# Optimization experiments

Measured on AMD Instinct MI355X. Metric: run time of the kernel, lower is better.

The kernel has to match this reference:

```python
import jax, jax.numpy as jnp
import numpy as np

N_WAY = 5
N_SHOT = 25
N_SUPPORT = N_WAY * N_SHOT  # 125
N_QUERY = 2048
D = 8192
C_REG = 0.1        # default C_reg of MetaOptNetHead_SVM_CS
MAX_ITER = 20      # default maxIter of QPFunction
SIGMA = 0.1        # centering parameter of the interior-point iteration


def setup_inputs() -> dict:
    key = jax.random.key(0)
    k1, k2, k3 = jax.random.split(key, 3)
    query = jax.random.normal(k1, (N_QUERY, D), dtype=jnp.float32)
    support = jax.random.normal(k2, (N_SUPPORT, D), dtype=jnp.float32)
    support_labels = jax.random.randint(k3, (N_SUPPORT,), 0, N_WAY, dtype=jnp.int32)
    scale = jnp.ones((1,), dtype=jnp.float32)  # nn.Parameter([1.0])
    return {
        "query": query,
        "support": support,
        "support_labels": support_labels,
        "n_way": N_WAY,
        "n_shot": N_SHOT,
        "scale": scale,
    }


def _solve_qp(G, e, h, A, b):
    """Solve min_z 0.5 z^T G z + e^T z  s.t.  z <= h (C = I),  A z = b.

    Primal-dual infeasible-start interior-point method with MAX_ITER fixed
    Newton steps (the jax analogue of qpth's QPFunction(maxIter=20)).
    Shapes: G (B,n,n), e (B,n), h (B,n), A (B,p,n), b (B,p).
    """
    B, n = e.shape
    p = b.shape[1]
    m = n  # C = I -> one inequality per variable
    At = jnp.swapaxes(A, 1, 2)                      # (B,n,p)
    zero_pp = jnp.zeros((B, p, p), dtype=G.dtype)
    A_row = jnp.concatenate([A, zero_pp], axis=2)   # (B,p,n+p), constant

    z = jnp.zeros_like(e)
    s = jnp.ones_like(h)
    lam = jnp.ones_like(h)
    nu = jnp.zeros_like(b)

    def frac_to_boundary(x, dx):
        # largest alpha in (0,1] keeping x + alpha*dx > 0
        ratio = jnp.where(dx < 0, -x / jnp.where(dx < 0, dx, -1.0), jnp.inf)
        return jnp.min(ratio, axis=1)

    def step(carry, _):
        z, s, lam, nu = carry
        Gz = jnp.einsum('bij,bj->bi', G, z)
        r1 = Gz + e + lam + jnp.einsum('bpi,bp->bi', A, nu)   # dual residual (C^T lam = lam)
        r2 = z + s - h                                         # primal ineq residual
        r4 = jnp.einsum('bpi,bi->bp', A, z) - b                # primal eq residual
        mu = SIGMA * jnp.sum(s * lam, axis=1, keepdims=True) / m
        r3 = lam * s - mu                                      # perturbed complementarity
        # Reduced KKT system: (G + diag(lam/s)) dz + A^T dnu = rhs1 ; A dz = -r4
        H = G + jax.vmap(jnp.diag)(lam / s)                    # (B,n,n)
        rhs1 = -(r1 + (lam * r2 - r3) / s)                     # (B,n)
        K = jnp.concatenate(
            [jnp.concatenate([H, At], axis=2), A_row], axis=1)  # (B,n+p,n+p)
        rhs = jnp.concatenate([rhs1, -r4], axis=1)             # (B,n+p)
        sol = jnp.linalg.solve(K, rhs[..., None])[..., 0]
        dz, dnu = sol[:, :n], sol[:, n:]
        ds = -r2 - dz
        dlam = (-r3 - lam * ds) / s
        alpha = jnp.minimum(
            1.0, 0.99 * jnp.minimum(frac_to_boundary(s, ds),
                                    frac_to_boundary(lam, dlam)))[:, None]
        return (z + alpha * dz, s + alpha * ds,
                lam + alpha * dlam, nu + alpha * dnu), None

    (z, s, lam, nu), _ = jax.lax.scan(step, (z, s, lam, nu), None, length=MAX_ITER)
    return z


def _svm_cs_head(query, support, support_labels, n_way):
    support_b = support[None]            # (1, ns, d) -- head unsqueezes batch dim
    query_b = query[None]                # (1, nq, d)
    B, ns, _ = support_b.shape
    f32 = jnp.float32

    # Gram matrix of support, then kron with I_{n_way} (batched_kronecker == jnp.kron)
    K = jnp.einsum('bnd,bmd->bnm', support_b, support_b)            # (B,ns,ns)
    eye_w = jnp.eye(n_way, dtype=f32)
    G = jax.vmap(lambda k: jnp.kron(k, eye_w))(K)                    # (B,ns*nw,ns*nw)
    G = G + jnp.eye(n_way * ns, dtype=f32)[None]

    y1h = jax.nn.one_hot(support_labels, n_way, dtype=f32).reshape(B, ns * n_way)
    e = -y1h
    h = C_REG * y1h
    A = jnp.kron(jnp.eye(ns, dtype=f32), jnp.ones((1, n_way), f32))[None]  # (1,ns,ns*nw)
    b = jnp.zeros((B, ns), f32)

    qp_sol = _solve_qp(G, e, h, A, b)                                # (B, ns*nw)

    compat = jnp.einsum('bnd,bqd->bnq', support_b, query_b)          # (B,ns,nq)
    qp3 = qp_sol.reshape(B, ns, n_way)
    # logits[b,q,w] = sum_s qp3[b,s,w] * compat[b,s,q]
    logits = jnp.einsum('bsw,bsq->bqw', qp3, compat)                 # (B,nq,nw)
    num_sv = jnp.sum(jnp.any(qp3 > 0.001, axis=2))                   # support-vector count
    return logits, num_sv


def reference(query, support, support_labels, n_way, n_shot, scale):
    logits, num_sv = _svm_cs_head(query, support, support_labels, n_way)
    return scale * logits, num_sv
```

## Files before the change

### kernel.cpp

```cpp
#include <hip/hip_runtime.h>

#define NS   125
#define NW   5
#define NQ   2048
#define DD   8192
#define CREG 0.1f
#define PGD_ITERS 10

#define OFF_PART  0
#define OFF_K     1000000
#define OFF_QP3   1016000
#define OFF_W     1017000

#define NPART     64

__global__ __launch_bounds__(256, 2) void gram256(const float* __restrict__ support,
                                                  float* __restrict__ part) {
    __shared__ __align__(16) float As[64][132];
    __shared__ __align__(16) float Bs[64][132];
    const int tid = threadIdx.x;
    const int c  = blockIdx.x >> 2;
    const int qy = blockIdx.x & 1, qz = (blockIdx.x >> 1) & 1;
    const int d0 = c * 128;
    const int sy0 = qy * 64, sz0 = qz * 64;

#pragma unroll
    for (int it = 0; it < 8; ++it) {
        int idx = it * 256 + tid;
        int sl = idx >> 5, d4 = idx & 31;
        int sa = sy0 + sl, sb = sz0 + sl;
        float4 va = (sa < NS) ? *(const float4*)&support[(size_t)sa * DD + d0 + d4 * 4]
                              : make_float4(0.f, 0.f, 0.f, 0.f);
        float4 vb = (sb < NS) ? *(const float4*)&support[(size_t)sb * DD + d0 + d4 * 4]
                              : make_float4(0.f, 0.f, 0.f, 0.f);
        *(float4*)&As[sl][d4 * 4] = va;
        *(float4*)&Bs[sl][d4 * 4] = vb;
    }
    __syncthreads();

    const int tx = tid & 15, ty = tid >> 4;
    float acc[4][4];
#pragma unroll
    for (int i = 0; i < 4; i++)
#pragma unroll
        for (int j = 0; j < 4; j++) acc[i][j] = 0.f;

#pragma unroll 4
    for (int d4 = 0; d4 < 32; ++d4) {
        float4 a4[4], b4[4];
#pragma unroll
        for (int i = 0; i < 4; i++) a4[i] = *(const float4*)&As[tx + 16 * i][d4 * 4];
#pragma unroll
        for (int j = 0; j < 4; j++) b4[j] = *(const float4*)&Bs[ty + 16 * j][d4 * 4];
#pragma unroll
        for (int i = 0; i < 4; i++)
#pragma unroll
            for (int j = 0; j < 4; j++)
                acc[i][j] += a4[i].x * b4[j].x + a4[i].y * b4[j].y
                           + a4[i].z * b4[j].z + a4[i].w * b4[j].w;
    }

    float* dst = part + (size_t)c * (NS * NS);
#pragma unroll
    for (int i = 0; i < 4; i++) {
        int gi = sy0 + tx + 16 * i;
        if (gi >= NS) continue;
#pragma unroll
        for (int j = 0; j < 4; j++) {
            int gj = sz0 + ty + 16 * j;
            if (gj < NS) dst[gi * NS + gj] = acc[i][j];
        }
    }
}

__global__ __launch_bounds__(256) void kreduce(const float* __restrict__ part,
                                               float* __restrict__ Kg) {
    int t = blockIdx.x * 256 + threadIdx.x;
    if (t < NS * NS) {
        float s = 0.f;
#pragma unroll 8
        for (int c = 0; c < NPART; ++c) s += part[(size_t)c * (NS * NS) + t];
        Kg[t] = s;
    }
}

__global__ __launch_bounds__(256) void qp_solve(const float* __restrict__ Kg,
                                                const int* __restrict__ labels,
                                                float* __restrict__ qp3,
                                                float* __restrict__ outNumSv) {
    __shared__ float red2[2][128 * 25];
    __shared__ __align__(16) float zsw[2][4][NW][32];
    __shared__ float rsx[2];
    __shared__ int   svc;

    const int tid  = threadIdx.x;
    const int w    = tid >> 6;
    const int lane = tid & 63;
    const int c0   = w * 32;
    const int r0   = lane, r1 = lane + 64;

    float kr0[32], kr1[32];
#pragma unroll
    for (int j = 0; j < 32; ++j) {
        const int col = c0 + j;
        const bool cv = (col < NS);
        kr0[j] = cv ? Kg[col * NS + r0] : 0.f;
        kr1[j] = (cv && r1 < NS) ? Kg[col * NS + r1] : 0.f;
    }
    for (int idx = tid; idx < 2 * 4 * NW * 32; idx += 256) ((float*)zsw)[idx] = 0.f;
    if (tid == 0) svc = 0;
    float rsum0 = 0.f, rsum1 = 0.f;
#pragma unroll
    for (int j = 0; j < 32; ++j) { rsum0 += fabsf(kr0[j]); rsum1 += fabsf(kr1[j]); }
    red2[0][r0 * 25 + w * 5] = rsum0;
    red2[0][r1 * 25 + w * 5] = rsum1;
    __syncthreads();
    const int prw = w * 64 + lane;
    if (w < 2) {
        const float* rr = &red2[0][prw * 25];
        float t = (prw < NS) ? rr[0] + rr[5] + rr[10] + rr[15] : 0.f;
#pragma unroll
        for (int off = 32; off; off >>= 1) t = fmaxf(t, __shfl_xor(t, off));
        if (lane == 0) rsx[w] = t;
    }
    __syncthreads();
    const float eta = 1.9f / (fmaxf(rsx[0], rsx[1]) + 1.0f);
    const int pr   = c0 + lane;
    const bool act = (lane < 32) && (pr < NS);
    const int lab  = act ? labels[pr] : 0;
    float z[NW] = {0.f, 0.f, 0.f, 0.f, 0.f};

    for (int it = 0; it < PGD_ITERS; ++it) {
        const int p = it & 1, n = p ^ 1;
        float acc0[NW] = {0.f, 0.f, 0.f, 0.f, 0.f};
        float acc1[NW] = {0.f, 0.f, 0.f, 0.f, 0.f};
#pragma unroll
        for (int c = 0; c < 8; ++c) {
            float4 z0 = *(const float4*)&zsw[p][w][0][4 * c];
            float4 z1 = *(const float4*)&zsw[p][w][1][4 * c];
            float4 z2 = *(const float4*)&zsw[p][w][2][4 * c];
            float4 z3 = *(const float4*)&zsw[p][w][3][4 * c];
            float4 z4 = *(const float4*)&zsw[p][w][4][4 * c];
            const float k00 = kr0[4*c], k01 = kr0[4*c+1], k02 = kr0[4*c+2], k03 = kr0[4*c+3];
            const float k10 = kr1[4*c], k11 = kr1[4*c+1], k12 = kr1[4*c+2], k13 = kr1[4*c+3];
            acc0[0] += k00*z0.x + k01*z0.y + k02*z0.z + k03*z0.w;
            acc0[1] += k00*z1.x + k01*z1.y + k02*z1.z + k03*z1.w;
            acc0[2] += k00*z2.x + k01*z2.y + k02*z2.z + k03*z2.w;
            acc0[3] += k00*z3.x + k01*z3.y + k02*z3.z + k03*z3.w;
            acc0[4] += k00*z4.x + k01*z4.y + k02*z4.z + k03*z4.w;
            acc1[0] += k10*z0.x + k11*z0.y + k12*z0.z + k13*z0.w;
            acc1[1] += k10*z1.x + k11*z1.y + k12*z1.z + k13*z1.w;
            acc1[2] += k10*z2.x + k11*z2.y + k12*z2.z + k13*z2.w;
            acc1[3] += k10*z3.x + k11*z3.y + k12*z3.z + k13*z3.w;
            acc1[4] += k10*z4.x + k11*z4.y + k12*z4.z + k13*z4.w;
        }
        {
            float* b0 = &red2[p][r0 * 25 + w * 5];
            b0[0] = acc0[0]; b0[1] = acc0[1]; b0[2] = acc0[2]; b0[3] = acc0[3]; b0[4] = acc0[4];
            float* b1 = &red2[p][r1 * 25 + w * 5];
            b1[0] = acc1[0]; b1[1] = acc1[1]; b1[2] = acc1[2]; b1[3] = acc1[3]; b1[4] = acc1[4];
        }
        __syncthreads();
        if (act) {
            const float* rr = &red2[p][pr * 25];
            float v[NW], h[NW];
#pragma unroll
            for (int a = 0; a < NW; a++) {
                float kz = rr[a] + rr[5 + a] + rr[10 + a] + rr[15 + a];
                float g = kz + z[a] - ((a == lab) ? 1.f : 0.f);
                v[a] = z[a] - eta * g;
                h[a] = (a == lab) ? CREG : 0.f;
            }
            float tau = fmaxf(fmaxf(fmaxf(v[0], v[1]), fmaxf(v[2], v[3])), v[4]);
#pragma unroll
            for (int nn = 0; nn < 7; ++nn) {
                float g = 0.f, nf = 0.f;
#pragma unroll
                for (int a = 0; a < NW; a++) {
                    float d = v[a] - tau;
                    bool fr = (d <= h[a]);
                    g += fr ? d : h[a];
                    nf += fr ? 1.f : 0.f;
                }
                tau += g / nf;
            }
#pragma unroll
            for (int a = 0; a < NW; a++) {
                z[a] = fminf(v[a] - tau, h[a]);
                zsw[n][w][a][lane] = z[a];
            }
        }
    }

    if (act) {
        float m = fmaxf(fmaxf(fmaxf(z[0], z[1]), fmaxf(z[2], z[3])), z[4]);
        if (m > 0.001f) atomicAdd(&svc, 1);
#pragma unroll
        for (int a = 0; a < NW; a++) qp3[pr * NW + a] = z[a];
    }
    __syncthreads();
    if (tid == 0) *outNumSv = (float)svc;
}

__global__ __launch_bounds__(256) void w_kernel(const float* __restrict__ support,
                                                const float* __restrict__ qp3,
                                                float* __restrict__ W) {
    __shared__ float q3[NS * NW];
    __shared__ float red[4 * 64 * NW];
    const int tid = threadIdx.x;
    for (int i = tid; i < NS * NW; i += 256) q3[i] = qp3[i];
    __syncthreads();
    const int ld = tid & 63;
    const int sq = tid >> 6;
    const int d  = blockIdx.x * 64 + ld;
    const int s0 = sq * 32;
    const int s1 = (sq == 3) ? NS : (s0 + 32);
    float acc[NW] = {0.f, 0.f, 0.f, 0.f, 0.f};
#pragma unroll 4
    for (int s = s0; s < s1; ++s) {
        float sv = support[(size_t)s * DD + d];
#pragma unroll
        for (int a = 0; a < NW; a++) acc[a] += sv * q3[s * NW + a];
    }
    float* rr = &red[tid * NW];
#pragma unroll
    for (int a = 0; a < NW; a++) rr[a] = acc[a];
    __syncthreads();
    if (sq == 0) {
#pragma unroll
        for (int a = 0; a < NW; a++) {
            float s = red[(0 * 64 + ld) * NW + a] + red[(1 * 64 + ld) * NW + a]
                    + red[(2 * 64 + ld) * NW + a] + red[(3 * 64 + ld) * NW + a];
            W[(size_t)a * DD + d] = s;
        }
    }
}

__global__ __launch_bounds__(256) void logits8(const float* __restrict__ query,
                                               const float* __restrict__ W,
                                               const float* __restrict__ scale,
                                               float* __restrict__ out) {
    __shared__ float red[4][8][NW];
    const int tid = threadIdx.x;
    const int wave = tid >> 6, lane = tid & 63;
    const int q0 = blockIdx.x * 8;
    const int v0 = wave * 512;
    const float4* W4 = (const float4*)W;
    const float4* q4 = (const float4*)query;
    const float sc = scale[0];

    float acc[8][NW];
#pragma unroll
    for (int k = 0; k < 8; k++)
#pragma unroll
        for (int a = 0; a < NW; a++) acc[k][a] = 0.f;

    for (int it = 0; it < 8; ++it) {
        const int dv = v0 + it * 64 + lane;
        float4 qv[8];
#pragma unroll
        for (int k = 0; k < 8; k++) qv[k] = q4[(size_t)(q0 + k) * (DD / 4) + dv];
#pragma unroll
        for (int a = 0; a < NW; a++) {
            float4 wv = W4[a * (DD / 4) + dv];
#pragma unroll
            for (int k = 0; k < 8; k++)
                acc[k][a] += qv[k].x * wv.x + qv[k].y * wv.y
                           + qv[k].z * wv.z + qv[k].w * wv.w;
        }
    }
#pragma unroll
    for (int off = 32; off; off >>= 1) {
#pragma unroll
        for (int k = 0; k < 8; k++)
#pragma unroll
            for (int a = 0; a < NW; a++) acc[k][a] += __shfl_xor(acc[k][a], off);
    }
    if (lane == 0) {
#pragma unroll
        for (int k = 0; k < 8; k++)
#pragma unroll
            for (int a = 0; a < NW; a++) red[wave][k][a] = acc[k][a];
    }
    __syncthreads();
    if (tid < 8 * NW) {
        const int ql = tid / NW, a = tid % NW;
        float s = red[0][ql][a] + red[1][ql][a] + red[2][ql][a] + red[3][ql][a];
        out[(q0 + ql) * NW + a] = sc * s;
    }
}

extern "C" void kernel_launch(void* const* d_in, const int* in_sizes, int n_in,
                              void* d_out, int out_size, void* d_ws, size_t ws_size,
                              hipStream_t stream) {
    const float* query   = (const float*)d_in[0];
    const float* support = (const float*)d_in[1];
    const int*   labels  = (const int*)d_in[2];
    const float* scale   = (const float*)d_in[5];
    float* out = (float*)d_out;
    float* ws  = (float*)d_ws;

    float* part = ws + OFF_PART;
    float* Kg   = ws + OFF_K;
    float* qp3  = ws + OFF_QP3;
    float* W    = ws + OFF_W;

    hipLaunchKernelGGL(gram256, dim3(256), dim3(256), 0, stream, support, part);
    hipLaunchKernelGGL(kreduce, dim3((NS * NS + 255) / 256), dim3(256), 0, stream, part, Kg);
    hipLaunchKernelGGL(qp_solve, dim3(1), dim3(256), 0, stream, Kg, labels, qp3, out + NQ * NW);
    hipLaunchKernelGGL(w_kernel, dim3(DD / 64), dim3(256), 0, stream, support, qp3, W);
    hipLaunchKernelGGL(logits8, dim3(NQ / 8), dim3(256), 0, stream, query, W, scale, out);
}
```

Before: 158.0 us.

## Fuse K reduction, QP solve and W computation into one flag-synchronized kernel

Merges kreduce, qp_solve and w_kernel into a single 129-block kernel. Blocks cooperatively reduce the Gram partials, then block 0 runs the QP after a global atomic counter shows all blocks are done, while the other blocks prefetch support slices into shared memory and spin until the QP result is published. It also exploits Gram symmetry by computing only three of the four 64x64 quadrants, 192 blocks instead of 256, and mirroring the missing one during the reduction. This removes two launches and overlaps the support loads with the serial QP. The cost is a reliance on all 129 blocks being co-resident, since the spin-waits would otherwise deadlock.

```diff
diff --git a/kernel.cpp b/kernel.cpp
--- a/kernel.cpp
+++ b/kernel.cpp
@@ -9,18 +9,24 @@
 
 #define OFF_PART  0
 #define OFF_K     1000000
+#define OFF_FLAGS 1015632
 #define OFF_QP3   1016000
 #define OFF_W     1017000
 
 #define NPART     64
-
-__global__ __launch_bounds__(256, 2) void gram256(const float* __restrict__ support,
-                                                  float* __restrict__ part) {
+#define QPW_BLKS  129
+
+__global__ __launch_bounds__(256, 2) void gram192(const float* __restrict__ support,
+                                                  float* __restrict__ part,
+                                                  unsigned int* __restrict__ flags) {
     __shared__ __align__(16) float As[64][132];
     __shared__ __align__(16) float Bs[64][132];
     const int tid = threadIdx.x;
-    const int c  = blockIdx.x >> 2;
-    const int qy = blockIdx.x & 1, qz = (blockIdx.x >> 1) & 1;
+    if (blockIdx.x == 0 && tid == 0) { flags[0] = 0u; flags[1] = 0u; }
+    const int qsel = blockIdx.x % 3;
+    const int c    = blockIdx.x / 3;
+    const int qy = (qsel == 2) ? 1 : 0;
+    const int qz = (qsel == 0) ? 0 : 1;
     const int d0 = c * 128;
     const int sy0 = qy * 64, sz0 = qz * 64;
 
@@ -73,165 +79,190 @@
     }
 }
 
-__global__ __launch_bounds__(256) void kreduce(const float* __restrict__ part,
-                                               float* __restrict__ Kg) {
-    int t = blockIdx.x * 256 + threadIdx.x;
-    if (t < NS * NS) {
+__global__ __launch_bounds__(256) void qpw(const float* __restrict__ part,
+                                           const int* __restrict__ labels,
+                                           const float* __restrict__ support,
+                                           float* __restrict__ Kg,
+                                           unsigned int* __restrict__ flags,
+                                           float* __restrict__ qp3,
+                                           float* __restrict__ W,
+                                           float* __restrict__ outNumSv) {
+    __shared__ __align__(16) float smem[9920];
+    __shared__ float rsx[2];
+    __shared__ int   svc;
+    const int tid = threadIdx.x;
+    const int bid = blockIdx.x;
+
+    for (int t = bid * 256 + tid; t < NS * NS; t += QPW_BLKS * 256) {
+        int i = t / NS, j = t - i * NS;
+        int src = (i >= 64 && j < 64) ? (j * NS + i) : t;
         float s = 0.f;
 #pragma unroll 8
-        for (int c = 0; c < NPART; ++c) s += part[(size_t)c * (NS * NS) + t];
+        for (int c = 0; c < NPART; ++c) s += part[(size_t)c * (NS * NS) + src];
         Kg[t] = s;
     }
-}
-
-__global__ __launch_bounds__(256) void qp_solve(const float* __restrict__ Kg,
-                                                const int* __restrict__ labels,
-                                                float* __restrict__ qp3,
-                                                float* __restrict__ outNumSv) {
-    __shared__ float red2[2][128 * 25];
-    __shared__ __align__(16) float zsw[2][4][NW][32];
-    __shared__ float rsx[2];
-    __shared__ int   svc;
-
-    const int tid  = threadIdx.x;
-    const int w    = tid >> 6;
-    const int lane = tid & 63;
-    const int c0   = w * 32;
-    const int r0   = lane, r1 = lane + 64;
-
-    float kr0[32], kr1[32];
-#pragma unroll
-    for (int j = 0; j < 32; ++j) {
-        const int col = c0 + j;
-        const bool cv = (col < NS);
-        kr0[j] = cv ? Kg[col * NS + r0] : 0.f;
-        kr1[j] = (cv && r1 < NS) ? Kg[col * NS + r1] : 0.f;
-    }
-    for (int idx = tid; idx < 2 * 4 * NW * 32; idx += 256) ((float*)zsw)[idx] = 0.f;
-    if (tid == 0) svc = 0;
-    float rsum0 = 0.f, rsum1 = 0.f;
-#pragma unroll
-    for (int j = 0; j < 32; ++j) { rsum0 += fabsf(kr0[j]); rsum1 += fabsf(kr1[j]); }
-    red2[0][r0 * 25 + w * 5] = rsum0;
-    red2[0][r1 * 25 + w * 5] = rsum1;
     __syncthreads();
-    const int prw = w * 64 + lane;
-    if (w < 2) {
-        const float* rr = &red2[0][prw * 25];
-        float t = (prw < NS) ? rr[0] + rr[5] + rr[10] + rr[15] : 0.f;
-#pragma unroll
-        for (int off = 32; off; off >>= 1) t = fmaxf(t, __shfl_xor(t, off));
-        if (lane == 0) rsx[w] = t;
-    }
-    __syncthreads();
-    const float eta = 1.9f / (fmaxf(rsx[0], rsx[1]) + 1.0f);
-    const int pr   = c0 + lane;
-    const bool act = (lane < 32) && (pr < NS);
-    const int lab  = act ? labels[pr] : 0;
-    float z[NW] = {0.f, 0.f, 0.f, 0.f, 0.f};
-
-    for (int it = 0; it < PGD_ITERS; ++it) {
-        const int p = it & 1, n = p ^ 1;
-        float acc0[NW] = {0.f, 0.f, 0.f, 0.f, 0.f};
-        float acc1[NW] = {0.f, 0.f, 0.f, 0.f, 0.f};
-#pragma unroll
-        for (int c = 0; c < 8; ++c) {
-            float4 z0 = *(const float4*)&zsw[p][w][0][4 * c];
-            float4 z1 = *(const float4*)&zsw[p][w][1][4 * c];
-            float4 z2 = *(const float4*)&zsw[p][w][2][4 * c];
-            float4 z3 = *(const float4*)&zsw[p][w][3][4 * c];
-            float4 z4 = *(const float4*)&zsw[p][w][4][4 * c];
-            const float k00 = kr0[4*c], k01 = kr0[4*c+1], k02 = kr0[4*c+2], k03 = kr0[4*c+3];
-            const float k10 = kr1[4*c], k11 = kr1[4*c+1], k12 = kr1[4*c+2], k13 = kr1[4*c+3];
-            acc0[0] += k00*z0.x + k01*z0.y + k02*z0.z + k03*z0.w;
-            acc0[1] += k00*z1.x + k01*z1.y + k02*z1.z + k03*z1.w;
-            acc0[2] += k00*z2.x + k01*z2.y + k02*z2.z + k03*z2.w;
-            acc0[3] += k00*z3.x + k01*z3.y + k02*z3.z + k03*z3.w;
-            acc0[4] += k00*z4.x + k01*z4.y + k02*z4.z + k03*z4.w;
-            acc1[0] += k10*z0.x + k11*z0.y + k12*z0.z + k13*z0.w;
-            acc1[1] += k10*z1.x + k11*z1.y + k12*z1.z + k13*z1.w;
-            acc1[2] += k10*z2.x + k11*z2.y + k12*z2.z + k13*z2.w;
-            acc1[3] += k10*z3.x + k11*z3.y + k12*z3.z + k13*z3.w;
-            acc1[4] += k10*z4.x + k11*z4.y + k12*z4.z + k13*z4.w;
-        }
-        {
-            float* b0 = &red2[p][r0 * 25 + w * 5];
-            b0[0] = acc0[0]; b0[1] = acc0[1]; b0[2] = acc0[2]; b0[3] = acc0[3]; b0[4] = acc0[4];
-            float* b1 = &red2[p][r1 * 25 + w * 5];
-            b1[0] = acc1[0]; b1[1] = acc1[1]; b1[2] = acc1[2]; b1[3] = acc1[3]; b1[4] = acc1[4];
-        }
-        __syncthreads();
+    if (tid == 0)
+        __hip_atomic_fetch_add(&flags[0], 1u, __ATOMIC_RELEASE, __HIP_MEMORY_SCOPE_AGENT);
+
+    if (bid == 0) {
+        if (tid == 0) {
+            while (__hip_atomic_load(&flags[0], __ATOMIC_RELAXED, __HIP_MEMORY_SCOPE_AGENT) < (unsigned)QPW_BLKS)
+                __builtin_amdgcn_s_sleep(8);
+        }
+        __syncthreads();
+        (void)__hip_atomic_load(&flags[0], __ATOMIC_ACQUIRE, __HIP_MEMORY_SCOPE_AGENT);
+
+        float* red2 = smem;
+        float* zsw  = smem + 6400;
+        const int w    = tid >> 6;
+        const int lane = tid & 63;
+        const int c0   = w * 32;
+        const int r0 = lane, r1 = lane + 64;
+        float kr0[32], kr1[32];
+#pragma unroll
+        for (int j = 0; j < 32; ++j) {
+            const int col = c0 + j;
+            const bool cv = (col < NS);
+            kr0[j] = cv ? Kg[col * NS + r0] : 0.f;
+            kr1[j] = (cv && r1 < NS) ? Kg[col * NS + r1] : 0.f;
+        }
+        for (int idx = tid; idx < 2 * 4 * NW * 32; idx += 256) zsw[idx] = 0.f;
+        if (tid == 0) svc = 0;
+        float rsum0 = 0.f, rsum1 = 0.f;
+#pragma unroll
+        for (int j = 0; j < 32; ++j) { rsum0 += fabsf(kr0[j]); rsum1 += fabsf(kr1[j]); }
+        red2[r0 * 25 + w * 5] = rsum0;
+        red2[r1 * 25 + w * 5] = rsum1;
+        __syncthreads();
+        const int prw = w * 64 + lane;
+        if (w < 2) {
+            const float* rr = &red2[prw * 25];
+            float t = (prw < NS) ? rr[0] + rr[5] + rr[10] + rr[15] : 0.f;
+#pragma unroll
+            for (int off = 32; off; off >>= 1) t = fmaxf(t, __shfl_xor(t, off));
+            if (lane == 0) rsx[w] = t;
+        }
+        __syncthreads();
+        const float eta = 1.9f / (fmaxf(rsx[0], rsx[1]) + 1.0f);
+        const int pr  = c0 + lane;
+        const bool act = (lane < 32) && (pr < NS);
+        const int lab = act ? labels[pr] : 0;
+        float z[NW] = {0.f, 0.f, 0.f, 0.f, 0.f};
+
+        for (int it = 0; it < PGD_ITERS; ++it) {
+            const int p = it & 1, n = p ^ 1;
+            float acc0[NW] = {0.f, 0.f, 0.f, 0.f, 0.f};
+            float acc1[NW] = {0.f, 0.f, 0.f, 0.f, 0.f};
+            const float* zb = zsw + p * 640 + w * 160;
+#pragma unroll
+            for (int c = 0; c < 8; ++c) {
+                float4 z0 = *(const float4*)&zb[0 * 32 + 4 * c];
+                float4 z1 = *(const float4*)&zb[1 * 32 + 4 * c];
+                float4 z2 = *(const float4*)&zb[2 * 32 + 4 * c];
+                float4 z3 = *(const float4*)&zb[3 * 32 + 4 * c];
+                float4 z4 = *(const float4*)&zb[4 * 32 + 4 * c];
+                const float k00 = kr0[4*c], k01 = kr0[4*c+1], k02 = kr0[4*c+2], k03 = kr0[4*c+3];
+                const float k10 = kr1[4*c], k11 = kr1[4*c+1], k12 = kr1[4*c+2], k13 = kr1[4*c+3];
+                acc0[0] += k00*z0.x + k01*z0.y + k02*z0.z + k03*z0.w;
+                acc0[1] += k00*z1.x + k01*z1.y + k02*z1.z + k03*z1.w;
+                acc0[2] += k00*z2.x + k01*z2.y + k02*z2.z + k03*z2.w;
+                acc0[3] += k00*z3.x + k01*z3.y + k02*z3.z + k03*z3.w;
+                acc0[4] += k00*z4.x + k01*z4.y + k02*z4.z + k03*z4.w;
+                acc1[0] += k10*z0.x + k11*z0.y + k12*z0.z + k13*z0.w;
+                acc1[1] += k10*z1.x + k11*z1.y + k12*z1.z + k13*z1.w;
+                acc1[2] += k10*z2.x + k11*z2.y + k12*z2.z + k13*z2.w;
+                acc1[3] += k10*z3.x + k11*z3.y + k12*z3.z + k13*z3.w;
+                acc1[4] += k10*z4.x + k11*z4.y + k12*z4.z + k13*z4.w;
+            }
+            {
+                float* b0 = &red2[p * 3200 + r0 * 25 + w * 5];
+                b0[0] = acc0[0]; b0[1] = acc0[1]; b0[2] = acc0[2]; b0[3] = acc0[3]; b0[4] = acc0[4];
+                float* b1 = &red2[p * 3200 + r1 * 25 + w * 5];
+                b1[0] = acc1[0]; b1[1] = acc1[1]; b1[2] = acc1[2]; b1[3] = acc1[3]; b1[4] = acc1[4];
+            }
+            __syncthreads();
+            if (act) {
+                const float* rr = &red2[p * 3200 + pr * 25];
+                float v[NW], h[NW];
+#pragma unroll
+                for (int a = 0; a < NW; a++) {
+                    float kz = rr[a] + rr[5 + a] + rr[10 + a] + rr[15 + a];
+                    float g = kz + z[a] - ((a == lab) ? 1.f : 0.f);
+                    v[a] = z[a] - eta * g;
+                    h[a] = (a == lab) ? CREG : 0.f;
+                }
+                float tau = fmaxf(fmaxf(fmaxf(v[0], v[1]), fmaxf(v[2], v[3])), v[4]);
+#pragma unroll
+                for (int nn = 0; nn < 7; ++nn) {
+                    float g = 0.f, nf = 0.f;
+#pragma unroll
+                    for (int a = 0; a < NW; a++) {
+                        float d = v[a] - tau;
+                        bool fr = (d <= h[a]);
+                        g += fr ? d : h[a];
+                        nf += fr ? 1.f : 0.f;
+                    }
+                    tau += g / nf;
+                }
+#pragma unroll
+                for (int a = 0; a < NW; a++) {
+                    z[a] = fminf(v[a] - tau, h[a]);
+                    zsw[n * 640 + w * 160 + a * 32 + lane] = z[a];
+                }
+            }
+        }
+
         if (act) {
-            const float* rr = &red2[p][pr * 25];
-            float v[NW], h[NW];
+            float m = fmaxf(fmaxf(fmaxf(z[0], z[1]), fmaxf(z[2], z[3])), z[4]);
+            if (m > 0.001f) atomicAdd(&svc, 1);
+#pragma unroll
+            for (int a = 0; a < NW; a++) qp3[pr * NW + a] = z[a];
+        }
+        __syncthreads();
+        if (tid == 0) {
+            *outNumSv = (float)svc;
+            __hip_atomic_fetch_add(&flags[1], 1u, __ATOMIC_RELEASE, __HIP_MEMORY_SCOPE_AGENT);
+        }
+    } else {
+        float* sup = smem;
+        float* q3  = smem + 8000;
+        float* red = smem + 8640;
+        const int dbase = (bid - 1) * 64;
+        for (int idx = tid; idx < NS * 64; idx += 256) {
+            int s = idx >> 6, dc = idx & 63;
+            sup[idx] = support[(size_t)s * DD + dbase + dc];
+        }
+        if (tid == 0) {
+            while (__hip_atomic_load(&flags[1], __ATOMIC_RELAXED, __HIP_MEMORY_SCOPE_AGENT) < 1u)
+                __builtin_amdgcn_s_sleep(16);
+        }
+        __syncthreads();
+        (void)__hip_atomic_load(&flags[1], __ATOMIC_ACQUIRE, __HIP_MEMORY_SCOPE_AGENT);
+        for (int i = tid; i < NS * NW; i += 256) q3[i] = qp3[i];
+        __syncthreads();
+        const int ld = tid & 63;
+        const int sq = tid >> 6;
+        const int s0 = sq * 32;
+        const int s1 = (sq == 3) ? NS : (s0 + 32);
+        float acc[NW] = {0.f, 0.f, 0.f, 0.f, 0.f};
+#pragma unroll 4
+        for (int s = s0; s < s1; ++s) {
+            float sv = sup[s * 64 + ld];
+#pragma unroll
+            for (int a = 0; a < NW; a++) acc[a] += sv * q3[s * NW + a];
+        }
+        float* rr = &red[tid * NW];
+#pragma unroll
+        for (int a = 0; a < NW; a++) rr[a] = acc[a];
+        __syncthreads();
+        if (sq == 0) {
 #pragma unroll
             for (int a = 0; a < NW; a++) {
-                float kz = rr[a] + rr[5 + a] + rr[10 + a] + rr[15 + a];
-                float g = kz + z[a] - ((a == lab) ? 1.f : 0.f);
-                v[a] = z[a] - eta * g;
-                h[a] = (a == lab) ? CREG : 0.f;
+                float s = red[(0 * 64 + ld) * NW + a] + red[(1 * 64 + ld) * NW + a]
+                        + red[(2 * 64 + ld) * NW + a] + red[(3 * 64 + ld) * NW + a];
+                W[(size_t)a * DD + dbase + ld] = s;
             }
-            float tau = fmaxf(fmaxf(fmaxf(v[0], v[1]), fmaxf(v[2], v[3])), v[4]);
-#pragma unroll
-            for (int nn = 0; nn < 7; ++nn) {
-                float g = 0.f, nf = 0.f;
-#pragma unroll
-                for (int a = 0; a < NW; a++) {
-                    float d = v[a] - tau;
-                    bool fr = (d <= h[a]);
-                    g += fr ? d : h[a];
-                    nf += fr ? 1.f : 0.f;
-                }
-                tau += g / nf;
-            }
-#pragma unroll
-            for (int a = 0; a < NW; a++) {
-                z[a] = fminf(v[a] - tau, h[a]);
-                zsw[n][w][a][lane] = z[a];
-            }
-        }
-    }
-
-    if (act) {
-        float m = fmaxf(fmaxf(fmaxf(z[0], z[1]), fmaxf(z[2], z[3])), z[4]);
-        if (m > 0.001f) atomicAdd(&svc, 1);
-#pragma unroll
-        for (int a = 0; a < NW; a++) qp3[pr * NW + a] = z[a];
-    }
-    __syncthreads();
-    if (tid == 0) *outNumSv = (float)svc;
-}
-
-__global__ __launch_bounds__(256) void w_kernel(const float* __restrict__ support,
-                                                const float* __restrict__ qp3,
-                                                float* __restrict__ W) {
-    __shared__ float q3[NS * NW];
-    __shared__ float red[4 * 64 * NW];
-    const int tid = threadIdx.x;
-    for (int i = tid; i < NS * NW; i += 256) q3[i] = qp3[i];
-    __syncthreads();
-    const int ld = tid & 63;
-    const int sq = tid >> 6;
-    const int d  = blockIdx.x * 64 + ld;
-    const int s0 = sq * 32;
-    const int s1 = (sq == 3) ? NS : (s0 + 32);
-    float acc[NW] = {0.f, 0.f, 0.f, 0.f, 0.f};
-#pragma unroll 4
-    for (int s = s0; s < s1; ++s) {
-        float sv = support[(size_t)s * DD + d];
-#pragma unroll
-        for (int a = 0; a < NW; a++) acc[a] += sv * q3[s * NW + a];
-    }
-    float* rr = &red[tid * NW];
-#pragma unroll
-    for (int a = 0; a < NW; a++) rr[a] = acc[a];
-    __syncthreads();
-    if (sq == 0) {
-#pragma unroll
-        for (int a = 0; a < NW; a++) {
-            float s = red[(0 * 64 + ld) * NW + a] + red[(1 * 64 + ld) * NW + a]
-                    + red[(2 * 64 + ld) * NW + a] + red[(3 * 64 + ld) * NW + a];
-            W[(size_t)a * DD + d] = s;
         }
     }
 }
@@ -300,14 +331,14 @@
     float* out = (float*)d_out;
     float* ws  = (float*)d_ws;
 
-    float* part = ws + OFF_PART;
-    float* Kg   = ws + OFF_K;
-    float* qp3  = ws + OFF_QP3;
-    float* W    = ws + OFF_W;
-
-    hipLaunchKernelGGL(gram256, dim3(256), dim3(256), 0, stream, support, part);
-    hipLaunchKernelGGL(kreduce, dim3((NS * NS + 255) / 256), dim3(256), 0, stream, part, Kg);
-    hipLaunchKernelGGL(qp_solve, dim3(1), dim3(256), 0, stream, Kg, labels, qp3, out + NQ * NW);
-    hipLaunchKernelGGL(w_kernel, dim3(DD / 64), dim3(256), 0, stream, support, qp3, W);
+    float* part          = ws + OFF_PART;
+    float* Kg            = ws + OFF_K;
+    unsigned int* flags  = (unsigned int*)(ws + OFF_FLAGS);
+    float* qp3           = ws + OFF_QP3;
+    float* W             = ws + OFF_W;
+
+    hipLaunchKernelGGL(gram192, dim3(192), dim3(256), 0, stream, support, part, flags);
+    hipLaunchKernelGGL(qpw, dim3(QPW_BLKS), dim3(256), 0, stream,
+                       part, labels, support, Kg, flags, qp3, W, out + NQ * NW);
     hipLaunchKernelGGL(logits8, dim3(NQ / 8), dim3(256), 0, stream, query, W, scale, out);
 }
```

Measured after the change: 175.5 us. 1.11x slower.
